# Optimization experiments

Hardware: AMD Instinct MI355X
Metric: run time of the kernel (lower is better)

The kernel has to match this reference:

```python
import jax, jax.numpy as jnp
import numpy as np

BUFFER_C = 1.25

def setup_inputs() -> dict:
    key = jax.random.key(0)
    k1, k2, k3 = jax.random.split(key, 3)
    T, D, E = 4096, 1024, 8
    x = jax.random.normal(k1, (T, D), dtype=jnp.float32)
    Wg = jax.random.normal(k2, (D, E), dtype=jnp.float32) / np.sqrt(D)
    bg = jnp.zeros((E,), dtype=jnp.float32)
    W = jax.random.normal(k3, (E, D, D), dtype=jnp.float32) / np.sqrt(D)
    b = jnp.zeros((E, D), dtype=jnp.float32)
    return {"x": x, "Wg": Wg, "bg": bg, "W": W, "b": b}


def reference(x, Wg, bg, W, b):
    # Top-1 (Switch-style) routing with capacity buffer, per-expert Linear,
    # prob-weighted combine, plus load-balancing aux loss.
    T, D = x.shape
    E = W.shape[0]
    capacity = int(BUFFER_C * T / E)

    logits = x @ Wg + bg                      # [T, E]
    probs = jax.nn.softmax(logits, axis=-1)   # [T, E]
    top_idx = jnp.argmax(probs, axis=-1)      # [T]
    top_prob = jnp.take_along_axis(probs, top_idx[:, None], axis=-1)[:, 0]

    onehot = jax.nn.one_hot(top_idx, E, dtype=x.dtype)       # [T, E]
    # 1-indexed position of each token within its expert's buffer
    pos = jnp.cumsum(onehot, axis=0) * onehot                # [T, E]
    dispatch = jnp.where((onehot > 0) & (pos <= capacity), 1.0, 0.0).astype(x.dtype)

    # dense dispatch/combine equivalent of the masked per-expert loop
    xe = jnp.einsum('te,td->etd', dispatch, x)               # [E, T, D]
    ye = jnp.einsum('etd,edf->etf', xe, W) + b[:, None, :]   # [E, T, D]
    y = jnp.einsum('te,etf->tf', dispatch, ye)               # [T, D] (0 for dropped)
    out = y * top_prob[:, None]

    # aux load-balance loss: E * sum_e f_e * P_e
    f = onehot.mean(axis=0)
    P = probs.mean(axis=0)
    aux_loss = E * jnp.sum(f * P)
    return out, aux_loss
```

## Files before the change

kernel.cpp:

```cpp
#include <hip/hip_runtime.h>
#include <hip/hip_bf16.h>
#include <cstdint>

#define T_TOK 4096
#define D_DIM 1024
#define E_EXP 8
#define CAP   640
#define NBIN  64
#define MAXDROP 3456
#define MT    10

typedef __attribute__((ext_vector_type(8))) short short8;
typedef __attribute__((ext_vector_type(4))) float f32x4;

__device__ inline unsigned short f2bf(float f) {
    uint32_t u = __float_as_uint(f);
    u += 0x7fffu + ((u >> 16) & 1u);
    return (unsigned short)(u >> 16);
}

__device__ inline void dma16(const void* g, void* l) {
    __builtin_amdgcn_global_load_lds(
        (const __attribute__((address_space(1))) unsigned int*)g,
        (__attribute__((address_space(3))) unsigned int*)l, 16, 0, 0);
}

#define WB_TILE(e, nt, kt) ((((size_t)(e) * 16 + (nt)) * 16 + (kt)) * 4096)
#define XG_TILE(e, mt, kt) ((((size_t)(e) * MT + (mt)) * 16 + (kt)) * 4096)

__global__ __launch_bounds__(256) void trans_kernel(
    const float* __restrict__ W, unsigned short* __restrict__ Wb,
    float* __restrict__ ppart)
{
    __shared__ unsigned short tile[64][66];
    int bid = blockIdx.x, tid = threadIdx.x;
    if (bid == 0) { ppart[tid] = 0.f; ppart[tid + 256] = 0.f; }

    int e  = bid >> 8;
    int kt = (bid >> 4) & 15;
    int nt = bid & 15;
    int k0 = kt * 64, n0 = nt * 64;
    const float* Wsrc = W + (size_t)e * D_DIM * D_DIM;
    #pragma unroll
    for (int p = 0; p < 4; p++) {
        int kk = p * 16 + (tid >> 4);
        int nn = (tid & 15) * 4;
        float4 v = *(const float4*)(Wsrc + (size_t)(k0 + kk) * D_DIM + n0 + nn);
        ushort4 u;
        u.x = f2bf(v.x); u.y = f2bf(v.y); u.z = f2bf(v.z); u.w = f2bf(v.w);
        *(ushort4*)&tile[kk][nn] = u;
    }
    __syncthreads();
    unsigned short* dst = Wb + WB_TILE(e, nt, kt);
    #pragma unroll
    for (int p = 0; p < 2; p++) {
        int c = tid + 256 * p;
        int g = c >> 6, n = c & 63;
        short8 v;
        #pragma unroll
        for (int z = 0; z < 8; z++) v[z] = (short)tile[g * 8 + z][n];
        *(short8*)&dst[(size_t)c * 8] = v;
    }
}

__global__ __launch_bounds__(1024) void gate_kernel(
    const float* __restrict__ x, const float* __restrict__ Wg,
    const float* __restrict__ bg,
    int* __restrict__ top_idx, float* __restrict__ top_prob, float* __restrict__ ppart)
{
    __shared__ float WgT[8][1024];
    int tid = threadIdx.x;
    {
        const float4* wr = (const float4*)(Wg + (size_t)tid * 8);
        float4 a = wr[0], bq = wr[1];
        WgT[0][tid] = a.x;  WgT[1][tid] = a.y;  WgT[2][tid] = a.z;  WgT[3][tid] = a.w;
        WgT[4][tid] = bq.x; WgT[5][tid] = bq.y; WgT[6][tid] = bq.z; WgT[7][tid] = bq.w;
    }
    __syncthreads();

    int wid  = tid >> 6;
    int lane = tid & 63;
    int t = blockIdx.x * 16 + wid;

    const float* xr = x + (size_t)t * D_DIM;
    float acc[8];
    #pragma unroll
    for (int e = 0; e < 8; e++) acc[e] = 0.f;

    #pragma unroll
    for (int ii = 0; ii < 8; ii++) {
        int da = lane + 128 * ii;
        int db = da + 64;
        float xa = xr[da];
        float xc = xr[db];
        #pragma unroll
        for (int e = 0; e < 8; e++)
            acc[e] += xa * WgT[e][da] + xc * WgT[e][db];
    }
    #pragma unroll
    for (int off = 32; off > 0; off >>= 1) {
        #pragma unroll
        for (int e = 0; e < 8; e++) acc[e] += __shfl_xor(acc[e], off, 64);
    }
    if (lane == 0) {
        float lg[8];
        #pragma unroll
        for (int e = 0; e < 8; e++) lg[e] = acc[e] + bg[e];
        float m = lg[0]; int am = 0;
        #pragma unroll
        for (int e = 1; e < 8; e++) { if (lg[e] > m) { m = lg[e]; am = e; } }
        float ex[8], s = 0.f;
        #pragma unroll
        for (int e = 0; e < 8; e++) { ex[e] = expf(lg[e] - m); s += ex[e]; }
        float inv = 1.f / s;
        top_idx[t]  = am;
        top_prob[t] = ex[am] * inv;
        int bin = (int)(blockIdx.x & (NBIN - 1));
        #pragma unroll
        for (int e = 0; e < 8; e++) atomicAdd(&ppart[bin * 8 + e], ex[e] * inv);
    }
}

__global__ __launch_bounds__(1024) void scan_kernel(
    const int* __restrict__ top_idx,
    int* __restrict__ tok_list, int* __restrict__ cnt,
    const float* __restrict__ ppart,
    float* __restrict__ out, float* __restrict__ out_aux)
{
    __shared__ int counts[64][8];
    __shared__ int excl[64][8];
    __shared__ int fulltot[8];
    __shared__ int droplist[MAXDROP];
    __shared__ int ndrop;

    int tid  = threadIdx.x;
    int wv   = tid >> 6;
    int lane = tid & 63;
    unsigned long long ltmask = (lane == 0) ? 0ull : ((~0ull) >> (64 - lane));

    if (tid == 0) ndrop = 0;

    int ecache[4];
    #pragma unroll
    for (int c = 0; c < 4; c++)
        ecache[c] = top_idx[(4 * wv + c) * 64 + lane];

    #pragma unroll
    for (int c = 0; c < 4; c++) {
        int chunk = 4 * wv + c;
        int e = ecache[c];
        #pragma unroll
        for (int q = 0; q < 8; q++) {
            unsigned long long mk = __ballot(e == q);
            int tot = __popcll(mk);
            if (lane == q) counts[chunk][q] = tot;
        }
    }
    __syncthreads();

    if (wv == 0) {
        #pragma unroll
        for (int q = 0; q < 8; q++) {
            int v = counts[lane][q];
            int orig = v;
            #pragma unroll
            for (int off = 1; off < 64; off <<= 1) {
                int n = __shfl_up(v, off, 64);
                if (lane >= off) v += n;
            }
            excl[lane][q] = v - orig;
            int total = __shfl(v, 63, 64);
            if (lane == 0) {
                fulltot[q] = total;
                cnt[q] = total < CAP ? total : CAP;
            }
        }
    }
    __syncthreads();

    #pragma unroll
    for (int c = 0; c < 4; c++) {
        int chunk = 4 * wv + c;
        int t = chunk * 64 + lane;
        int e = ecache[c];
        int pos = 0;
        #pragma unroll
        for (int q = 0; q < 8; q++) {
            unsigned long long mk = __ballot(e == q);
            if (e == q) pos = excl[chunk][q] + __popcll(mk & ltmask);
        }
        if (pos < CAP) {
            tok_list[e * CAP + pos] = t;
        } else {
            int di = atomicAdd(&ndrop, 1);
            droplist[di] = t;
        }
    }
    __syncthreads();

    int nd = ndrop;
    int grp = tid >> 8;
    int col = (tid & 255) * 4;
    float4 z = {0.f, 0.f, 0.f, 0.f};
    for (int d = grp; d < nd; d += 4) {
        int row = droplist[d];
        *(float4*)&out[(size_t)row * D_DIM + col] = z;
    }

    if (wv == 0) {
        float p[8];
        #pragma unroll
        for (int e = 0; e < 8; e++) p[e] = ppart[lane * 8 + e];
        #pragma unroll
        for (int off = 32; off > 0; off >>= 1) {
            #pragma unroll
            for (int e = 0; e < 8; e++) p[e] += __shfl_xor(p[e], off, 64);
        }
        if (lane == 0) {
            float s = 0.f;
            #pragma unroll
            for (int e = 0; e < 8; e++)
                s += ((float)fulltot[e] / (float)T_TOK) * (p[e] / (float)T_TOK);
            out_aux[0] = (float)E_EXP * s;
        }
    }
}

__global__ __launch_bounds__(256) void gather_kernel(
    const float* __restrict__ x, const int* __restrict__ tok_list,
    const int* __restrict__ cnt, unsigned short* __restrict__ xg)
{
    int bid = blockIdx.x;
    int e   = bid / 40;
    int rem = bid % 40;
    int mt  = rem >> 2, ktg = rem & 3;
    int count = cnt[e];
    int m0 = mt * 64;
    if (m0 >= count) return;

    int tid = threadIdx.x;
    const int* tl = tok_list + e * CAP;

    #pragma unroll
    for (int kk = 0; kk < 4; kk++) {
        int kt = ktg * 4 + kk;
        unsigned short* dst = xg + XG_TILE(e, mt, kt);
        #pragma unroll
        for (int p = 0; p < 2; p++) {
            int c = tid + 256 * p;
            int g = c >> 6, row = c & 63;
            int gm = m0 + row;
            int tok = tl[gm < count ? gm : count - 1];
            const float* src = x + (size_t)tok * D_DIM + kt * 64 + g * 8;
            float4 v0 = *(const float4*)(src);
            float4 v1 = *(const float4*)(src + 4);
            short8 v;
            v[0] = f2bf(v0.x); v[1] = f2bf(v0.y); v[2] = f2bf(v0.z); v[3] = f2bf(v0.w);
            v[4] = f2bf(v1.x); v[5] = f2bf(v1.y); v[6] = f2bf(v1.z); v[7] = f2bf(v1.w);
            *(short8*)&dst[(size_t)c * 8] = v;
        }
    }
}

__global__ __launch_bounds__(256) void expert_gemm(
    const unsigned short* __restrict__ xg, const unsigned short* __restrict__ Wb,
    const float* __restrict__ bias,
    const int* __restrict__ tok_list, const int* __restrict__ cnt,
    const float* __restrict__ top_prob, float* __restrict__ out)
{
    int bid = blockIdx.x;
    int e   = bid / 40;
    int rem = bid % 40;
    int mtt = rem >> 3, ntt = rem & 7;
    int count = cnt[e];
    int m0 = mtt * 128;
    if (m0 >= count) return;
    int n0 = ntt * 128;

    __shared__ unsigned short Ab[2][16][64][8];
    __shared__ unsigned short Bb[2][16][64][8];

    int tid  = threadIdx.x;
    int lane = tid & 63, w = tid >> 6;
    int quad = lane >> 4, l16 = lane & 15;
    int mh = w >> 1;
    int nh = w & 1;
    size_t lo = (size_t)lane * 8;

    const int* tl = tok_list + e * CAP;
    const unsigned short* A0 = xg + XG_TILE(e, mtt * 2, 0) + lo;
    const unsigned short* A1 = xg + XG_TILE(e, mtt * 2 + 1, 0) + lo;
    const unsigned short* B0 = Wb + WB_TILE(e, ntt * 2, 0) + lo;
    const unsigned short* B1 = Wb + WB_TILE(e, ntt * 2 + 1, 0) + lo;

    f32x4 acc[4][4];
    #pragma unroll
    for (int i = 0; i < 4; i++)
        #pragma unroll
        for (int j = 0; j < 4; j++)
            acc[i][j] = (f32x4){0.f, 0.f, 0.f, 0.f};

    auto stage = [&](int kt, int buf) {
        const unsigned short* a0 = A0 + (size_t)kt * 4096;
        const unsigned short* a1 = A1 + (size_t)kt * 4096;
        const unsigned short* b0 = B0 + (size_t)kt * 4096;
        const unsigned short* b1 = B1 + (size_t)kt * 4096;
        #pragma unroll
        for (int d = 0; d < 8; d++) {
            int g = w + 4 * d;
            if (g < 8)        dma16(a0 + (size_t)g * 512,        &Ab[buf][g][0][0]);
            else if (g < 16)  dma16(a1 + (size_t)(g - 8) * 512,  &Ab[buf][g][0][0]);
            else if (g < 24)  dma16(b0 + (size_t)(g - 16) * 512, &Bb[buf][g - 16][0][0]);
            else              dma16(b1 + (size_t)(g - 24) * 512, &Bb[buf][g - 16][0][0]);
        }
    };

    stage(0, 0);
    int cur = 0;
    #pragma unroll 1
    for (int kt = 0; kt < 16; kt++) {
        __syncthreads();
        if (kt + 1 < 16) stage(kt + 1, cur ^ 1);

        #pragma unroll
        for (int s = 0; s < 2; s++) {
            int g = s * 4 + quad;
            short8 af[4], bf[4];
            #pragma unroll
            for (int i = 0; i < 4; i++)
                af[i] = *(const short8*)&Ab[cur][mh * 8 + g][16 * i + l16][0];
            #pragma unroll
            for (int j = 0; j < 4; j++)
                bf[j] = *(const short8*)&Bb[cur][nh * 8 + g][16 * j + l16][0];
            #pragma unroll
            for (int i = 0; i < 4; i++)
                #pragma unroll
                for (int j = 0; j < 4; j++)
                    acc[i][j] = __builtin_amdgcn_mfma_f32_16x16x32_bf16(
                        af[i], bf[j], acc[i][j], 0, 0, 0);
        }
        cur ^= 1;
    }

    float bv[4];
    #pragma unroll
    for (int j = 0; j < 4; j++)
        bv[j] = bias[e * D_DIM + n0 + nh * 64 + 16 * j + l16];

    #pragma unroll
    for (int i = 0; i < 4; i++) {
        int rb = m0 + mh * 64 + 16 * i + quad * 4;
        #pragma unroll
        for (int r = 0; r < 4; r++) {
            int gm = rb + r;
            if (gm >= count) continue;
            int tok = tl[gm];
            float p = top_prob[tok];
            float* orow = out + (size_t)tok * D_DIM + n0 + nh * 64 + l16;
            #pragma unroll
            for (int j = 0; j < 4; j++)
                orow[16 * j] = (acc[i][j][r] + bv[j]) * p;
        }
    }
}

extern "C" void kernel_launch(void* const* d_in, const int* in_sizes, int n_in,
                              void* d_out, int out_size, void* d_ws, size_t ws_size,
                              hipStream_t stream) {
    const float* x  = (const float*)d_in[0];
    const float* Wg = (const float*)d_in[1];
    const float* bg = (const float*)d_in[2];
    const float* W  = (const float*)d_in[3];
    const float* b  = (const float*)d_in[4];
    float* out = (float*)d_out;

    char* ws = (char*)d_ws;
    unsigned short* Wb = (unsigned short*)(ws + 0);
    unsigned short* xg = (unsigned short*)(ws + 16777216);
    int*   top_idx  = (int*)(ws + 27262976);
    float* top_prob = (float*)(ws + 27279360);
    int*   tok_list = (int*)(ws + 27295744);
    int*   cnt      = (int*)(ws + 27316224);
    float* ppart    = (float*)(ws + 27316256);

    hipLaunchKernelGGL(trans_kernel, dim3(2048), dim3(256), 0, stream, W, Wb, ppart);
    hipLaunchKernelGGL(gate_kernel, dim3(T_TOK / 16), dim3(1024), 0, stream,
                       x, Wg, bg, top_idx, top_prob, ppart);
    hipLaunchKernelGGL(scan_kernel, dim3(1), dim3(1024), 0, stream,
                       top_idx, tok_list, cnt, ppart, out, out + (size_t)T_TOK * D_DIM);
    hipLaunchKernelGGL(gather_kernel, dim3(320), dim3(256), 0, stream,
                       x, tok_list, cnt, xg);
    hipLaunchKernelGGL(expert_gemm, dim3(E_EXP * 5 * 8), dim3(256), 0, stream,
                       xg, Wb, b, tok_list, cnt, top_prob, out);
}
```

Baseline: 169.1 us.

## Fuse front-end stages into one cooperative kernel with grid syncs

```diff
diff --git a/kernel.cpp b/kernel.cpp
--- a/kernel.cpp
+++ b/kernel.cpp
@@ -1,12 +1,14 @@
 #include <hip/hip_runtime.h>
 #include <hip/hip_bf16.h>
+#include <hip/hip_cooperative_groups.h>
 #include <cstdint>
+
+namespace cg = cooperative_groups;
 
 #define T_TOK 4096
 #define D_DIM 1024
 #define E_EXP 8
 #define CAP   640
-#define NBIN  64
 #define MAXDROP 3456
 #define MT    10
 
@@ -28,236 +30,251 @@
 #define WB_TILE(e, nt, kt) ((((size_t)(e) * 16 + (nt)) * 16 + (kt)) * 4096)
 #define XG_TILE(e, mt, kt) ((((size_t)(e) * MT + (mt)) * 16 + (kt)) * 4096)
 
-__global__ __launch_bounds__(256) void trans_kernel(
-    const float* __restrict__ W, unsigned short* __restrict__ Wb,
-    float* __restrict__ ppart)
+__global__ __launch_bounds__(1024) void fused_front(
+    const float* __restrict__ x, const float* __restrict__ Wg,
+    const float* __restrict__ bg, const float* __restrict__ W,
+    unsigned short* __restrict__ Wb, unsigned short* __restrict__ xg,
+    int* __restrict__ top_idx, float* __restrict__ top_prob,
+    int* __restrict__ tok_list, int* __restrict__ cnt,
+    float* __restrict__ ppart,
+    float* __restrict__ out, float* __restrict__ out_aux)
 {
-    __shared__ unsigned short tile[64][66];
-    int bid = blockIdx.x, tid = threadIdx.x;
-    if (bid == 0) { ppart[tid] = 0.f; ppart[tid + 256] = 0.f; }
-
-    int e  = bid >> 8;
-    int kt = (bid >> 4) & 15;
-    int nt = bid & 15;
-    int k0 = kt * 64, n0 = nt * 64;
-    const float* Wsrc = W + (size_t)e * D_DIM * D_DIM;
-    #pragma unroll
-    for (int p = 0; p < 4; p++) {
-        int kk = p * 16 + (tid >> 4);
-        int nn = (tid & 15) * 4;
-        float4 v = *(const float4*)(Wsrc + (size_t)(k0 + kk) * D_DIM + n0 + nn);
-        ushort4 u;
-        u.x = f2bf(v.x); u.y = f2bf(v.y); u.z = f2bf(v.z); u.w = f2bf(v.w);
-        *(ushort4*)&tile[kk][nn] = u;
-    }
-    __syncthreads();
-    unsigned short* dst = Wb + WB_TILE(e, nt, kt);
-    #pragma unroll
-    for (int p = 0; p < 2; p++) {
-        int c = tid + 256 * p;
-        int g = c >> 6, n = c & 63;
-        short8 v;
-        #pragma unroll
-        for (int z = 0; z < 8; z++) v[z] = (short)tile[g * 8 + z][n];
-        *(short8*)&dst[(size_t)c * 8] = v;
-    }
-}
-
-__global__ __launch_bounds__(1024) void gate_kernel(
-    const float* __restrict__ x, const float* __restrict__ Wg,
-    const float* __restrict__ bg,
-    int* __restrict__ top_idx, float* __restrict__ top_prob, float* __restrict__ ppart)
-{
-    __shared__ float WgT[8][1024];
-    int tid = threadIdx.x;
+    __shared__ union {
+        unsigned short tile4[4][64][66];
+        float WgT[8][1024];
+        struct {
+            int counts[64][8];
+            int excl[64][8];
+            int fulltot[8];
+            float pred[16][8];
+            int droplist[MAXDROP];
+            int ndrop;
+        } sc;
+    } u;
+
+    cg::grid_group grid = cg::this_grid();
+    int bid  = blockIdx.x;
+    int tid  = threadIdx.x;
+    int wv   = tid >> 6;
+    int lane = tid & 63;
+    int ltid = tid & 255;
+    int sub  = tid >> 8;
+
+    #pragma unroll 1
+    for (int it = 0; it < 2; it++) {
+        int tile_id = bid * 8 + it * 4 + sub;
+        int e  = tile_id >> 8;
+        int kt = (tile_id >> 4) & 15;
+        int nt = tile_id & 15;
+        int k0 = kt * 64, n0 = nt * 64;
+        const float* Wsrc = W + (size_t)e * D_DIM * D_DIM;
+        #pragma unroll
+        for (int p = 0; p < 4; p++) {
+            int kk = p * 16 + (ltid >> 4);
+            int nn = (ltid & 15) * 4;
+            float4 v = *(const float4*)(Wsrc + (size_t)(k0 + kk) * D_DIM + n0 + nn);
+            ushort4 uq;
+            uq.x = f2bf(v.x); uq.y = f2bf(v.y); uq.z = f2bf(v.z); uq.w = f2bf(v.w);
+            *(ushort4*)&u.tile4[sub][kk][nn] = uq;
+        }
+        __syncthreads();
+        unsigned short* dst = Wb + WB_TILE(e, nt, kt);
+        #pragma unroll
+        for (int p = 0; p < 2; p++) {
+            int c = ltid + 256 * p;
+            int g = c >> 6, n = c & 63;
+            short8 v;
+            #pragma unroll
+            for (int z = 0; z < 8; z++) v[z] = (short)u.tile4[sub][g * 8 + z][n];
+            *(short8*)&dst[(size_t)c * 8] = v;
+        }
+        __syncthreads();
+    }
+
     {
         const float4* wr = (const float4*)(Wg + (size_t)tid * 8);
         float4 a = wr[0], bq = wr[1];
-        WgT[0][tid] = a.x;  WgT[1][tid] = a.y;  WgT[2][tid] = a.z;  WgT[3][tid] = a.w;
-        WgT[4][tid] = bq.x; WgT[5][tid] = bq.y; WgT[6][tid] = bq.z; WgT[7][tid] = bq.w;
+        u.WgT[0][tid] = a.x;  u.WgT[1][tid] = a.y;  u.WgT[2][tid] = a.z;  u.WgT[3][tid] = a.w;
+        u.WgT[4][tid] = bq.x; u.WgT[5][tid] = bq.y; u.WgT[6][tid] = bq.z; u.WgT[7][tid] = bq.w;
     }
     __syncthreads();
-
-    int wid  = tid >> 6;
-    int lane = tid & 63;
-    int t = blockIdx.x * 16 + wid;
-
-    const float* xr = x + (size_t)t * D_DIM;
-    float acc[8];
-    #pragma unroll
-    for (int e = 0; e < 8; e++) acc[e] = 0.f;
-
-    #pragma unroll
-    for (int ii = 0; ii < 8; ii++) {
-        int da = lane + 128 * ii;
-        int db = da + 64;
-        float xa = xr[da];
-        float xc = xr[db];
-        #pragma unroll
-        for (int e = 0; e < 8; e++)
-            acc[e] += xa * WgT[e][da] + xc * WgT[e][db];
-    }
-    #pragma unroll
-    for (int off = 32; off > 0; off >>= 1) {
-        #pragma unroll
-        for (int e = 0; e < 8; e++) acc[e] += __shfl_xor(acc[e], off, 64);
-    }
-    if (lane == 0) {
-        float lg[8];
-        #pragma unroll
-        for (int e = 0; e < 8; e++) lg[e] = acc[e] + bg[e];
-        float m = lg[0]; int am = 0;
-        #pragma unroll
-        for (int e = 1; e < 8; e++) { if (lg[e] > m) { m = lg[e]; am = e; } }
-        float ex[8], s = 0.f;
-        #pragma unroll
-        for (int e = 0; e < 8; e++) { ex[e] = expf(lg[e] - m); s += ex[e]; }
-        float inv = 1.f / s;
-        top_idx[t]  = am;
-        top_prob[t] = ex[am] * inv;
-        int bin = (int)(blockIdx.x & (NBIN - 1));
-        #pragma unroll
-        for (int e = 0; e < 8; e++) atomicAdd(&ppart[bin * 8 + e], ex[e] * inv);
-    }
-}
-
-__global__ __launch_bounds__(1024) void scan_kernel(
-    const int* __restrict__ top_idx,
-    int* __restrict__ tok_list, int* __restrict__ cnt,
-    const float* __restrict__ ppart,
-    float* __restrict__ out, float* __restrict__ out_aux)
-{
-    __shared__ int counts[64][8];
-    __shared__ int excl[64][8];
-    __shared__ int fulltot[8];
-    __shared__ int droplist[MAXDROP];
-    __shared__ int ndrop;
-
-    int tid  = threadIdx.x;
-    int wv   = tid >> 6;
-    int lane = tid & 63;
-    unsigned long long ltmask = (lane == 0) ? 0ull : ((~0ull) >> (64 - lane));
-
-    if (tid == 0) ndrop = 0;
-
-    int ecache[4];
-    #pragma unroll
-    for (int c = 0; c < 4; c++)
-        ecache[c] = top_idx[(4 * wv + c) * 64 + lane];
-
-    #pragma unroll
-    for (int c = 0; c < 4; c++) {
-        int chunk = 4 * wv + c;
-        int e = ecache[c];
-        #pragma unroll
-        for (int q = 0; q < 8; q++) {
-            unsigned long long mk = __ballot(e == q);
-            int tot = __popcll(mk);
-            if (lane == q) counts[chunk][q] = tot;
-        }
-    }
-    __syncthreads();
-
-    if (wv == 0) {
-        #pragma unroll
-        for (int q = 0; q < 8; q++) {
-            int v = counts[lane][q];
-            int orig = v;
-            #pragma unroll
-            for (int off = 1; off < 64; off <<= 1) {
-                int n = __shfl_up(v, off, 64);
-                if (lane >= off) v += n;
-            }
-            excl[lane][q] = v - orig;
-            int total = __shfl(v, 63, 64);
-            if (lane == 0) {
-                fulltot[q] = total;
-                cnt[q] = total < CAP ? total : CAP;
-            }
-        }
-    }
-    __syncthreads();
-
-    #pragma unroll
-    for (int c = 0; c < 4; c++) {
-        int chunk = 4 * wv + c;
-        int t = chunk * 64 + lane;
-        int e = ecache[c];
-        int pos = 0;
-        #pragma unroll
-        for (int q = 0; q < 8; q++) {
-            unsigned long long mk = __ballot(e == q);
-            if (e == q) pos = excl[chunk][q] + __popcll(mk & ltmask);
-        }
-        if (pos < CAP) {
-            tok_list[e * CAP + pos] = t;
-        } else {
-            int di = atomicAdd(&ndrop, 1);
-            droplist[di] = t;
-        }
-    }
-    __syncthreads();
-
-    int nd = ndrop;
-    int grp = tid >> 8;
-    int col = (tid & 255) * 4;
-    float4 z = {0.f, 0.f, 0.f, 0.f};
-    for (int d = grp; d < nd; d += 4) {
-        int row = droplist[d];
-        *(float4*)&out[(size_t)row * D_DIM + col] = z;
-    }
-
-    if (wv == 0) {
+    {
+        int t = bid * 16 + wv;
+        const float* xr = x + (size_t)t * D_DIM;
+        float acc[8];
+        #pragma unroll
+        for (int e = 0; e < 8; e++) acc[e] = 0.f;
+        #pragma unroll
+        for (int ii = 0; ii < 8; ii++) {
+            int da = lane + 128 * ii;
+            int db = da + 64;
+            float xa = xr[da];
+            float xc = xr[db];
+            #pragma unroll
+            for (int e = 0; e < 8; e++)
+                acc[e] += xa * u.WgT[e][da] + xc * u.WgT[e][db];
+        }
+        #pragma unroll
+        for (int off = 32; off > 0; off >>= 1) {
+            #pragma unroll
+            for (int e = 0; e < 8; e++) acc[e] += __shfl_xor(acc[e], off, 64);
+        }
+        if (lane == 0) {
+            float lg[8];
+            #pragma unroll
+            for (int e = 0; e < 8; e++) lg[e] = acc[e] + bg[e];
+            float m = lg[0]; int am = 0;
+            #pragma unroll
+            for (int e = 1; e < 8; e++) { if (lg[e] > m) { m = lg[e]; am = e; } }
+            float ex[8], s = 0.f;
+            #pragma unroll
+            for (int e = 0; e < 8; e++) { ex[e] = expf(lg[e] - m); s += ex[e]; }
+            float inv = 1.f / s;
+            top_idx[t]  = am;
+            top_prob[t] = ex[am] * inv;
+            float* pp = ppart + (size_t)t * 8;
+            #pragma unroll
+            for (int e = 0; e < 8; e++) pp[e] = ex[e] * inv;
+        }
+    }
+
+    grid.sync();
+
+    if (bid == 0) {
+        unsigned long long ltmask = (lane == 0) ? 0ull : ((~0ull) >> (64 - lane));
+        if (tid == 0) u.sc.ndrop = 0;
+
+        int ecache[4];
+        #pragma unroll
+        for (int c = 0; c < 4; c++)
+            ecache[c] = top_idx[(4 * wv + c) * 64 + lane];
+
+        #pragma unroll
+        for (int c = 0; c < 4; c++) {
+            int chunk = 4 * wv + c;
+            int e = ecache[c];
+            #pragma unroll
+            for (int q = 0; q < 8; q++) {
+                unsigned long long mk = __ballot(e == q);
+                int tot = __popcll(mk);
+                if (lane == q) u.sc.counts[chunk][q] = tot;
+            }
+        }
+        __syncthreads();
+
+        if (wv == 0) {
+            #pragma unroll
+            for (int q = 0; q < 8; q++) {
+                int v = u.sc.counts[lane][q];
+                int orig = v;
+                #pragma unroll
+                for (int off = 1; off < 64; off <<= 1) {
+                    int n = __shfl_up(v, off, 64);
+                    if (lane >= off) v += n;
+                }
+                u.sc.excl[lane][q] = v - orig;
+                int total = __shfl(v, 63, 64);
+                if (lane == 0) {
+                    u.sc.fulltot[q] = total;
+                    cnt[q] = total < CAP ? total : CAP;
+                }
+            }
+        }
+        __syncthreads();
+
+        #pragma unroll
+        for (int c = 0; c < 4; c++) {
+            int chunk = 4 * wv + c;
+            int t = chunk * 64 + lane;
+            int e = ecache[c];
+            int pos = 0;
+            #pragma unroll
+            for (int q = 0; q < 8; q++) {
+                unsigned long long mk = __ballot(e == q);
+                if (e == q) pos = u.sc.excl[chunk][q] + __popcll(mk & ltmask);
+            }
+            if (pos < CAP) {
+                tok_list[e * CAP + pos] = t;
+            } else {
+                int di = atomicAdd(&u.sc.ndrop, 1);
+                u.sc.droplist[di] = t;
+            }
+        }
+        __syncthreads();
+
+        int nd = u.sc.ndrop;
+        int grp = tid >> 8;
+        int col = (tid & 255) * 4;
+        float4 z = {0.f, 0.f, 0.f, 0.f};
+        for (int d = grp; d < nd; d += 4) {
+            int row = u.sc.droplist[d];
+            *(float4*)&out[(size_t)row * D_DIM + col] = z;
+        }
+
         float p[8];
         #pragma unroll
-        for (int e = 0; e < 8; e++) p[e] = ppart[lane * 8 + e];
+        for (int e = 0; e < 8; e++) p[e] = 0.f;
+        #pragma unroll
+        for (int i = 0; i < 4; i++) {
+            const float* pr = ppart + ((size_t)(tid * 4 + i)) * 8;
+            #pragma unroll
+            for (int e = 0; e < 8; e++) p[e] += pr[e];
+        }
         #pragma unroll
         for (int off = 32; off > 0; off >>= 1) {
             #pragma unroll
             for (int e = 0; e < 8; e++) p[e] += __shfl_xor(p[e], off, 64);
         }
         if (lane == 0) {
+            #pragma unroll
+            for (int e = 0; e < 8; e++) u.sc.pred[wv][e] = p[e];
+        }
+        __syncthreads();
+        if (tid == 0) {
             float s = 0.f;
             #pragma unroll
-            for (int e = 0; e < 8; e++)
-                s += ((float)fulltot[e] / (float)T_TOK) * (p[e] / (float)T_TOK);
+            for (int e = 0; e < 8; e++) {
+                float pe = 0.f;
+                #pragma unroll
+                for (int w16 = 0; w16 < 16; w16++) pe += u.sc.pred[w16][e];
+                s += ((float)u.sc.fulltot[e] / (float)T_TOK) * (pe / (float)T_TOK);
+            }
             out_aux[0] = (float)E_EXP * s;
         }
     }
-}
-
-__global__ __launch_bounds__(256) void gather_kernel(
-    const float* __restrict__ x, const int* __restrict__ tok_list,
-    const int* __restrict__ cnt, unsigned short* __restrict__ xg)
-{
-    int bid = blockIdx.x;
-    int e   = bid / 40;
-    int rem = bid % 40;
-    int mt  = rem >> 2, ktg = rem & 3;
-    int count = cnt[e];
-    int m0 = mt * 64;
-    if (m0 >= count) return;
-
-    int tid = threadIdx.x;
-    const int* tl = tok_list + e * CAP;
-
-    #pragma unroll
-    for (int kk = 0; kk < 4; kk++) {
-        int kt = ktg * 4 + kk;
-        unsigned short* dst = xg + XG_TILE(e, mt, kt);
-        #pragma unroll
-        for (int p = 0; p < 2; p++) {
-            int c = tid + 256 * p;
-            int g = c >> 6, row = c & 63;
-            int gm = m0 + row;
-            int tok = tl[gm < count ? gm : count - 1];
-            const float* src = x + (size_t)tok * D_DIM + kt * 64 + g * 8;
-            float4 v0 = *(const float4*)(src);
-            float4 v1 = *(const float4*)(src + 4);
-            short8 v;
-            v[0] = f2bf(v0.x); v[1] = f2bf(v0.y); v[2] = f2bf(v0.z); v[3] = f2bf(v0.w);
-            v[4] = f2bf(v1.x); v[5] = f2bf(v1.y); v[6] = f2bf(v1.z); v[7] = f2bf(v1.w);
-            *(short8*)&dst[(size_t)c * 8] = v;
+
+    grid.sync();
+
+    {
+        int unit = bid * 4 + sub;
+        if (unit < 320) {
+            int e   = unit / 40;
+            int rem = unit % 40;
+            int mt  = rem >> 2, ktg = rem & 3;
+            int count = cnt[e];
+            int m0 = mt * 64;
+            if (m0 < count) {
+                const int* tl = tok_list + e * CAP;
+                #pragma unroll
+                for (int kk = 0; kk < 4; kk++) {
+                    int kt = ktg * 4 + kk;
+                    unsigned short* dst = xg + XG_TILE(e, mt, kt);
+                    #pragma unroll
+                    for (int p = 0; p < 2; p++) {
+                        int c = ltid + 256 * p;
+                        int g = c >> 6, row = c & 63;
+                        int gm = m0 + row;
+                        int tok = tl[gm < count ? gm : count - 1];
+                        const float* src = x + (size_t)tok * D_DIM + kt * 64 + g * 8;
+                        float4 v0 = *(const float4*)(src);
+                        float4 v1 = *(const float4*)(src + 4);
+                        short8 v;
+                        v[0] = f2bf(v0.x); v[1] = f2bf(v0.y); v[2] = f2bf(v0.z); v[3] = f2bf(v0.w);
+                        v[4] = f2bf(v1.x); v[5] = f2bf(v1.y); v[6] = f2bf(v1.z); v[7] = f2bf(v1.w);
+                        *(short8*)&dst[(size_t)c * 8] = v;
+                    }
+                }
+            }
         }
     }
 }
@@ -382,14 +399,16 @@
     int*   tok_list = (int*)(ws + 27295744);
     int*   cnt      = (int*)(ws + 27316224);
     float* ppart    = (float*)(ws + 27316256);
-
-    hipLaunchKernelGGL(trans_kernel, dim3(2048), dim3(256), 0, stream, W, Wb, ppart);
-    hipLaunchKernelGGL(gate_kernel, dim3(T_TOK / 16), dim3(1024), 0, stream,
-                       x, Wg, bg, top_idx, top_prob, ppart);
-    hipLaunchKernelGGL(scan_kernel, dim3(1), dim3(1024), 0, stream,
-                       top_idx, tok_list, cnt, ppart, out, out + (size_t)T_TOK * D_DIM);
-    hipLaunchKernelGGL(gather_kernel, dim3(320), dim3(256), 0, stream,
-                       x, tok_list, cnt, xg);
+    float* out_aux  = out + (size_t)T_TOK * D_DIM;
+
+    void* args[] = {
+        (void*)&x, (void*)&Wg, (void*)&bg, (void*)&W,
+        (void*)&Wb, (void*)&xg, (void*)&top_idx, (void*)&top_prob,
+        (void*)&tok_list, (void*)&cnt, (void*)&ppart,
+        (void*)&out, (void*)&out_aux
+    };
+    hipLaunchCooperativeKernel((void*)fused_front, dim3(256), dim3(1024),
+                               args, 0, stream);
     hipLaunchKernelGGL(expert_gemm, dim3(E_EXP * 5 * 8), dim3(256), 0, stream,
                        xg, Wb, b, tok_list, cnt, top_prob, out);
 }
```

After: 216.8 us. 28.2% more time.
